# Kernel optimization log

Hardware: AMD Instinct MI355X
Metric: run time of the kernel (lower is better)

## Reference

```python
import jax, jax.numpy as jnp
import numpy as np


def _make_grid(h, w, stride=1):
    """Vectorized port of gen_grid_coordinates_exp. Returns (1, 3*Ho, 3*Wo, 2) float32,
    last dim = (x_norm, y_norm) in [-1,1] (torch grid_sample convention)."""
    rows = np.arange(0, h, stride)
    cols = np.arange(0, w, stride)
    theta = -((rows + 0.5) / h * np.pi - np.pi / 2)          # (Ho,)
    phi = (cols + 0.5) / w * 2 * np.pi - np.pi               # (Wo,)
    dtheta = np.pi / h
    dphi = 2 * np.pi / w
    # 3x3 tangent-plane offsets (du: horizontal, dv: vertical), per get_exp_duv
    du = np.tan(dphi) * np.array([[-1., 0., 1.]] * 3)                      # (3,3)
    dv = np.tan(dtheta) * np.array([[1., 1., 1.], [0., 0., 0.], [-1., -1., -1.]])
    T = theta[:, None, None, None]   # (Ho,1,1,1)
    P = phi[None, :, None, None]     # (1,Wo,1,1)
    u_x = -du * np.sin(P) - dv * np.sin(T) * np.cos(P)       # (Ho,Wo,3,3)
    u_y = du * np.cos(P) - dv * np.sin(T) * np.sin(P)
    u_z = dv * np.cos(T) + np.zeros_like(u_x)
    u_norm = np.sqrt(u_x ** 2 + u_y ** 2 + u_z ** 2)
    u_div = np.where(u_norm == 0, 1.0, u_norm)
    c, s = np.cos(u_norm), np.sin(u_norm)
    ex = np.cos(T) * np.cos(P) * c + u_x / u_div * s
    ey = np.cos(T) * np.sin(P) * c + u_y / u_div * s
    ez = np.sin(T) * c + u_z / u_div * s
    new_phi = np.arctan2(ey, ex)
    new_theta = np.arcsin(np.clip(ez, -1.0, 1.0))
    new_r = (-new_theta + np.pi / 2) * h / np.pi - 0.5
    new_c = ((new_phi + np.pi) * w / (2 * np.pi) - 0.5 + w) % w
    # kernel center samples the original integer pixel exactly
    new_r[:, :, 1, 1] = rows[:, None]
    new_c[:, :, 1, 1] = cols[None, :]
    gx = new_c * 2.0 / w - 1.0
    gy = new_r * 2.0 / h - 1.0
    grid = np.stack([gx, gy], axis=-1)                        # (Ho,Wo,3,3,2)
    Ho, Wo = len(rows), len(cols)
    grid = grid.transpose(0, 2, 1, 3, 4).reshape(1, Ho * 3, Wo * 3, 2)
    return grid.astype(np.float32)


def _grid_sample_bilinear(x, grid):
    """torch.nn.functional.grid_sample(mode='bilinear', padding='zeros', align_corners=False).
    x: (B,C,H,W); grid: (1,Hg,Wg,2) shared across batch."""
    B, C, H, W = x.shape
    gx = grid[0, ..., 0]
    gy = grid[0, ..., 1]
    Hg, Wg = gx.shape
    ix = ((gx + 1.0) * W - 1.0) * 0.5   # unnormalize, align_corners=False
    iy = ((gy + 1.0) * H - 1.0) * 0.5
    x0 = jnp.floor(ix); x1 = x0 + 1.0
    y0 = jnp.floor(iy); y1 = y0 + 1.0
    xf = x.reshape(B, C, H * W)

    def corner(xc, yc, wgt):
        valid = (xc >= 0) & (xc < W) & (yc >= 0) & (yc < H)
        xi = jnp.clip(xc, 0, W - 1).astype(jnp.int32)
        yi = jnp.clip(yc, 0, H - 1).astype(jnp.int32)
        idx = (yi * W + xi).reshape(-1)                      # (Hg*Wg,)
        w_eff = (wgt * valid.astype(wgt.dtype)).reshape(-1)  # zero-pad OOB
        return xf[:, :, idx] * w_eff                          # (B,C,Hg*Wg)

    out = (corner(x0, y0, (x1 - ix) * (y1 - iy))
           + corner(x1, y0, (ix - x0) * (y1 - iy))
           + corner(x0, y1, (x1 - ix) * (iy - y0))
           + corner(x1, y1, (ix - x0) * (iy - y0)))
    return out.reshape(B, C, Hg, Wg)


def setup_inputs() -> dict:
    key = jax.random.key(0)
    k1, k2 = jax.random.split(key)
    B, Cin, Cout, H, W = 4, 128, 256, 128, 256
    x = jax.random.normal(k1, (B, Cin, H, W), dtype=jnp.float32)
    # kaiming_uniform_(a=sqrt(5)) -> U(-1/sqrt(fan_in), 1/sqrt(fan_in)), fan_in = Cin*9
    bound = 1.0 / np.sqrt(Cin * 9)
    weight = jax.random.uniform(k2, (Cout, Cin, 3, 3), dtype=jnp.float32,
                                minval=-bound, maxval=bound)
    bias = jnp.zeros((Cout,), dtype=jnp.float32)
    grid = jnp.asarray(_make_grid(H, W, stride=1))  # (1, 3H, 3W, 2)
    return {"x": x, "weight": weight, "bias": bias, "grid": grid}


def reference(x, weight, bias, grid):
    sampled = _grid_sample_bilinear(x, grid)                 # (B,C,3H,3W)
    out = jax.lax.conv_general_dilated(
        sampled, weight, window_strides=(3, 3), padding='VALID',
        dimension_numbers=('NCHW', 'OIHW', 'NCHW'))          # (B,Cout,H,W)
    return out + bias[None, :, None, None]
```

## Files before the change

kernel.cpp:

```cpp
#include <hip/hip_runtime.h>


#define Hh   128
#define Ww   256
#define HWp  (Hh*Ww)
#define CIN  128
#define COUT 256
#define KTOT 1152
#define NPTS (384*768)
#define BM   64
#define BN   256
#define BK   32
#define NKS  (KTOT/BK)

typedef __attribute__((ext_vector_type(8))) _Float16 f16x8;
typedef __attribute__((ext_vector_type(4))) float    f32x4;

__device__ __forceinline__ f16x8 bcast8(float f) {
    _Float16 h = (_Float16)f;
    f16x8 v;
#pragma unroll
    for (int i = 0; i < 8; ++i) v[i] = h;
    return v;
}

__global__ void prep(const float* __restrict__ grid, const float* __restrict__ w,
                     const float* __restrict__ x,
                     int2* __restrict__ tI, float4* __restrict__ tW,
                     _Float16* __restrict__ wt2, _Float16* __restrict__ xt) {
    const int bid = blockIdx.x;
    const int t   = threadIdx.x;
    if (bid < NPTS / 256) {
        int g = bid * 256 + t;
        int hh = g / 768, ww = g - hh * 768;
        int ho = hh / 3, ii = hh - 3 * ho;
        int wo = ww / 3, jj = ww - 3 * wo;

        float gx = grid[2 * g + 0];
        float gy = grid[2 * g + 1];
        float ix = ((gx + 1.0f) * (float)Ww - 1.0f) * 0.5f;
        float iy = ((gy + 1.0f) * (float)Hh - 1.0f) * 0.5f;
        float x0f = floorf(ix), y0f = floorf(iy);
        int x0 = (int)x0f, y0 = (int)y0f;
        float wx1 = ix - x0f, wx0 = 1.0f - wx1;
        float wy1 = iy - y0f, wy0 = 1.0f - wy1;

        float wyt = (y0 >= 0 && y0 < Hh) ? wy0 : 0.0f;
        float wyb = (y0 + 1 >= 0 && y0 + 1 < Hh) ? wy1 : 0.0f;
        int r0 = min(max(y0, 0), Hh - 1);
        int r1 = min(max(y0 + 1, 0), Hh - 1);

        int xb; float cw0, cw1;
        if (x0 < 0)            { xb = 0;      cw0 = wx1; cw1 = 0.0f; }
        else if (x0 > Ww - 2)  { xb = Ww - 2; cw0 = 0.0f; cw1 = wx0; }
        else                   { xb = x0;     cw0 = wx0; cw1 = wx1; }

        int e = (ho * Ww + wo) * 9 + ii * 3 + jj;
        tI[e] = make_int2(r0 * Ww + xb, r1 * Ww + xb);
        tW[e] = make_float4(cw0 * wyt, cw1 * wyt, cw0 * wyb, cw1 * wyb);
    } else if (bid < 2 * (NPTS / 256)) {
        int o = (bid - NPTS / 256) * 256 + t;
        int kk = o & (BK - 1);
        int n  = (o >> 5) & (COUT - 1);
        int ks = o >> 13;
        int ij = ks % 9;
        int ci = (ks / 9) * 32 + kk;
        wt2[o] = (_Float16)w[n * KTOT + ci * 9 + ij];
    } else {
        int r   = (bid - 2 * (NPTS / 256)) * 256 + t;
        int sp4 = (r & 8191) * 4;
        int cg  = (r >> 13) & 15;
        int b   = r >> 17;
        const float* src = x + ((size_t)(b * CIN + cg * 8)) * HWp + sp4;
        float4 v[8];
#pragma unroll
        for (int j = 0; j < 8; ++j) v[j] = *(const float4*)(src + (size_t)j * HWp);
#pragma unroll
        for (int s = 0; s < 4; ++s) {
            f16x8 ov;
#pragma unroll
            for (int j = 0; j < 8; ++j) ov[j] = (_Float16)((&v[j].x)[s]);
            *(f16x8*)&xt[((size_t)(b * HWp + sp4 + s)) * CIN + cg * 8] = ov;
        }
    }
}

__global__ __launch_bounds__(512, 4) void sphconv_gemm(
    const _Float16* __restrict__ xt, const _Float16* __restrict__ wt2,
    const float* __restrict__ bias, const int2* __restrict__ tI,
    const float4* __restrict__ tW, float* __restrict__ out) {

    __shared__ int2   sTI[9 * BM];
    __shared__ float4 sTW[9 * BM];
    __shared__ __align__(16) _Float16 sA[2][BM * 40];

    const int t = threadIdx.x;
    const int bid = blockIdx.x;
    const int swz = (bid & 7) * 256 + (bid >> 3);
    const int m0  = swz * BM;
    const int b   = m0 >> 15;
    const int sp0 = m0 & (HWp - 1);
    const _Float16* xb_ = xt + (size_t)b * (HWp * CIN);

    for (int e = t; e < 9 * BM; e += 512) {
        int r = e & (BM - 1), ij = e >> 6;
        sTI[e] = tI[(sp0 + r) * 9 + ij];
        sTW[e] = tW[(sp0 + r) * 9 + ij];
    }

    const int lane = t & 63;
    const int wid  = t >> 6;
    const int wrow = wid >> 2;
    const int wcol = wid & 3;
    const int quad = lane >> 4;
    const int l16  = lane & 15;

    const bool isA = (t < 256);
    const int  mr  = t & 63;
    const int  chb = ((t >> 6) & 3) * 8;

    const _Float16* wfrag = wt2 + (wcol * 64 + l16) * BK + quad * 8;

    f32x4 acc[2][4];
#pragma unroll
    for (int r = 0; r < 2; ++r)
#pragma unroll
        for (int c = 0; c < 4; ++c) {
            f32x4 z = {0.0f, 0.0f, 0.0f, 0.0f};
            acc[r][c] = z;
        }

    __syncthreads();

    f16x8 bc[4], bn[4];
    if (isA) {
        const int2   o  = sTI[mr];
        const float4 wv = sTW[mr];
        const _Float16* p = xb_ + (size_t)o.x * CIN + chb;
        const _Float16* q = xb_ + (size_t)o.y * CIN + chb;
        f16x8 av = (*(const f16x8*)p)         * bcast8(wv.x)
                 + (*(const f16x8*)(p + CIN)) * bcast8(wv.y)
                 + (*(const f16x8*)q)         * bcast8(wv.z)
                 + (*(const f16x8*)(q + CIN)) * bcast8(wv.w);
        *(f16x8*)&sA[0][mr * 40 + chb] = av;
    }
#pragma unroll
    for (int c = 0; c < 4; ++c)
        bc[c] = *(const f16x8*)(wfrag + c * 16 * BK);
    __syncthreads();

#define STEP_BODY(KS, CURA, NXTA, BCUR, BNXT)                                   \
    {                                                                           \
        const int  ks_   = (KS);                                                \
        const bool have_ = (ks_ + 1 < NKS);                                     \
        f16x8 p00, p01, p10, p11;                                               \
        float4 wv;                                                              \
        if (isA && have_) {                                                     \
            const int ij2 = (ks_ + 1) % 9;                                      \
            const int cb2 = ((ks_ + 1) / 9) * 32;                               \
            const int2 o = sTI[ij2 * BM + mr];                                  \
            wv = sTW[ij2 * BM + mr];                                            \
            const _Float16* p = xb_ + (size_t)o.x * CIN + cb2 + chb;            \
            const _Float16* q = xb_ + (size_t)o.y * CIN + cb2 + chb;            \
            p00 = *(const f16x8*)p;  p01 = *(const f16x8*)(p + CIN);            \
            p10 = *(const f16x8*)q;  p11 = *(const f16x8*)(q + CIN);            \
        }                                                                       \
        if (have_) {                                                            \
            const _Float16* src = wfrag + (size_t)(ks_ + 1) * (COUT * BK);      \
            _Pragma("unroll")                                                   \
            for (int c = 0; c < 4; ++c)                                         \
                BNXT[c] = *(const f16x8*)(src + c * 16 * BK);                   \
        }                                                                       \
        f16x8 af[2];                                                            \
        _Pragma("unroll")                                                       \
        for (int r = 0; r < 2; ++r)                                             \
            af[r] = *(const f16x8*)(&CURA[(wrow * 32 + r * 16 + l16) * 40 +     \
                                          quad * 8]);                           \
        _Pragma("unroll")                                                       \
        for (int r = 0; r < 2; ++r)                                             \
            _Pragma("unroll")                                                   \
            for (int c = 0; c < 4; ++c)                                         \
                acc[r][c] = __builtin_amdgcn_mfma_f32_16x16x32_f16(             \
                    af[r], BCUR[c], acc[r][c], 0, 0, 0);                        \
        if (isA && have_) {                                                     \
            f16x8 av = p00 * bcast8(wv.x) + p01 * bcast8(wv.y)                  \
                     + p10 * bcast8(wv.z) + p11 * bcast8(wv.w);                 \
            *(f16x8*)&NXTA[mr * 40 + chb] = av;                                 \
        }                                                                       \
        __syncthreads();                                                        \
    }

    for (int ks = 0; ks < NKS; ks += 2) {
        STEP_BODY(ks,     sA[0], sA[1], bc, bn)
        STEP_BODY(ks + 1, sA[1], sA[0], bn, bc)
    }
#undef STEP_BODY

#pragma unroll
    for (int c = 0; c < 4; ++c) {
        int n = wcol * 64 + c * 16 + l16;
        float bv = bias[n];
        float* outn = out + (((size_t)(b * COUT + n)) << 15) + sp0;
#pragma unroll
        for (int r = 0; r < 2; ++r) {
            int mbase = wrow * 32 + r * 16 + quad * 4;
            float4 v = make_float4(acc[r][c][0] + bv, acc[r][c][1] + bv,
                                   acc[r][c][2] + bv, acc[r][c][3] + bv);
            *(float4*)(&outn[mbase]) = v;
        }
    }
}

extern "C" void kernel_launch(void* const* d_in, const int* in_sizes, int n_in,
                              void* d_out, int out_size, void* d_ws, size_t ws_size,
                              hipStream_t stream) {
    const float* x    = (const float*)d_in[0];
    const float* w    = (const float*)d_in[1];
    const float* bias = (const float*)d_in[2];
    const float* grid = (const float*)d_in[3];
    float* out = (float*)d_out;

    char* ws = (char*)d_ws;
    int2*     tI  = (int2*)(ws);
    float4*   tW  = (float4*)(ws + 2359296);
    _Float16* wt2 = (_Float16*)(ws + 7077888);
    _Float16* xt  = (_Float16*)(ws + 7667712);

    prep<<<1152 + 1152 + 2048, 256, 0, stream>>>(grid, w, x, tI, tW, wt2, xt);
    sphconv_gemm<<<(4 * HWp) / BM, 512, 0, stream>>>(xt, wt2, bias, tI, tW, out);
}
```

Measured before the change: 485.6 us.

## Double K-step per barrier and remap warps to full-M tiles

The GEMM main loop now handles two BK=32 slices per barrier, with a 64x72 shared A tile, so the number of __syncthreads is halved. All 512 threads gather A (each thread group takes one of the two k-slices), where before only half did. Each warp now owns all 64 rows and a 32-column slice of N, reading four A fragments from LDS per k-half. A manual lgkmcnt wait with s_barrier and sched_barrier replaces __syncthreads. The cost is more registers for prefetched B and A, and more LDS reads per warp.

```diff
diff --git a/kernel.cpp b/kernel.cpp
--- a/kernel.cpp
+++ b/kernel.cpp
@@ -12,6 +12,7 @@
 #define BN   256
 #define BK   32
 #define NKS  (KTOT/BK)
+#define NSS  (NKS/2)
 
 typedef __attribute__((ext_vector_type(8))) _Float16 f16x8;
 typedef __attribute__((ext_vector_type(4))) float    f32x4;
@@ -92,7 +93,7 @@
 
     __shared__ int2   sTI[9 * BM];
     __shared__ float4 sTW[9 * BM];
-    __shared__ __align__(16) _Float16 sA[2][BM * 40];
+    __shared__ __align__(16) _Float16 sA[2][BM * 72];
 
     const int t = threadIdx.x;
     const int bid = blockIdx.x;
@@ -110,100 +111,107 @@
 
     const int lane = t & 63;
     const int wid  = t >> 6;
-    const int wrow = wid >> 2;
-    const int wcol = wid & 3;
+    const int wcol = wid;
     const int quad = lane >> 4;
     const int l16  = lane & 15;
-
-    const bool isA = (t < 256);
-    const int  mr  = t & 63;
-    const int  chb = ((t >> 6) & 3) * 8;
-
-    const _Float16* wfrag = wt2 + (wcol * 64 + l16) * BK + quad * 8;
-
-    f32x4 acc[2][4];
-#pragma unroll
-    for (int r = 0; r < 2; ++r)
-#pragma unroll
-        for (int c = 0; c < 4; ++c) {
+    const int qk   = quad * 8;
+
+    const int row = t & 63;
+    const int chb = ((t >> 6) & 3) * 8;
+    const int g   = t >> 8;
+
+    const int wb = (wcol * 32 + l16) * BK + qk;
+
+    f32x4 acc[4][2];
+#pragma unroll
+    for (int r = 0; r < 4; ++r)
+#pragma unroll
+        for (int c = 0; c < 2; ++c) {
             f32x4 z = {0.0f, 0.0f, 0.0f, 0.0f};
             acc[r][c] = z;
         }
 
     __syncthreads();
 
-    f16x8 bc[4], bn[4];
-    if (isA) {
-        const int2   o  = sTI[mr];
-        const float4 wv = sTW[mr];
+    f16x8 bcA[4], bcB[4];
+    {
+        const int2   o  = sTI[g * BM + row];
+        const float4 wv = sTW[g * BM + row];
         const _Float16* p = xb_ + (size_t)o.x * CIN + chb;
         const _Float16* q = xb_ + (size_t)o.y * CIN + chb;
         f16x8 av = (*(const f16x8*)p)         * bcast8(wv.x)
                  + (*(const f16x8*)(p + CIN)) * bcast8(wv.y)
                  + (*(const f16x8*)q)         * bcast8(wv.z)
                  + (*(const f16x8*)(q + CIN)) * bcast8(wv.w);
-        *(f16x8*)&sA[0][mr * 40 + chb] = av;
-    }
-#pragma unroll
-    for (int c = 0; c < 4; ++c)
-        bc[c] = *(const f16x8*)(wfrag + c * 16 * BK);
+        *(f16x8*)&sA[0][row * 72 + g * 32 + chb] = av;
+        const _Float16* ws0 = wt2 + wb;
+        bcA[0] = *(const f16x8*)(ws0);
+        bcA[1] = *(const f16x8*)(ws0 + 16 * BK);
+        bcA[2] = *(const f16x8*)(ws0 + COUT * BK);
+        bcA[3] = *(const f16x8*)(ws0 + COUT * BK + 16 * BK);
+    }
     __syncthreads();
 
-#define STEP_BODY(KS, CURA, NXTA, BCUR, BNXT)                                   \
+#define SUPER(S, CUR, NXT, BC, BN)                                              \
     {                                                                           \
-        const int  ks_   = (KS);                                                \
-        const bool have_ = (ks_ + 1 < NKS);                                     \
+        const bool have_ = ((S) + 1 < NSS);                                     \
         f16x8 p00, p01, p10, p11;                                               \
-        float4 wv;                                                              \
-        if (isA && have_) {                                                     \
-            const int ij2 = (ks_ + 1) % 9;                                      \
-            const int cb2 = ((ks_ + 1) / 9) * 32;                               \
-            const int2 o = sTI[ij2 * BM + mr];                                  \
-            wv = sTW[ij2 * BM + mr];                                            \
-            const _Float16* p = xb_ + (size_t)o.x * CIN + cb2 + chb;            \
-            const _Float16* q = xb_ + (size_t)o.y * CIN + cb2 + chb;            \
+        float4 wvn;                                                             \
+        if (have_) {                                                            \
+            const int mk  = 2 * ((S) + 1) + g;                                  \
+            const int ijn = mk % 9;                                             \
+            const int cbn = (mk / 9) * 32;                                      \
+            const int2 o  = sTI[ijn * BM + row];                                \
+            wvn = sTW[ijn * BM + row];                                          \
+            const _Float16* p = xb_ + (size_t)o.x * CIN + cbn + chb;            \
+            const _Float16* q = xb_ + (size_t)o.y * CIN + cbn + chb;            \
             p00 = *(const f16x8*)p;  p01 = *(const f16x8*)(p + CIN);            \
             p10 = *(const f16x8*)q;  p11 = *(const f16x8*)(q + CIN);            \
+            const _Float16* ws_ = wt2 + (size_t)(2 * ((S) + 1)) * (COUT * BK)   \
+                                      + wb;                                     \
+            BN[0] = *(const f16x8*)(ws_);                                       \
+            BN[1] = *(const f16x8*)(ws_ + 16 * BK);                             \
+            BN[2] = *(const f16x8*)(ws_ + COUT * BK);                           \
+            BN[3] = *(const f16x8*)(ws_ + COUT * BK + 16 * BK);                 \
+        }                                                                       \
+        _Pragma("unroll")                                                       \
+        for (int kh = 0; kh < 2; ++kh) {                                        \
+            f16x8 af[4];                                                        \
+            _Pragma("unroll")                                                   \
+            for (int r = 0; r < 4; ++r)                                         \
+                af[r] = *(const f16x8*)(&CUR[(r * 16 + l16) * 72 +              \
+                                             kh * 32 + qk]);                    \
+            _Pragma("unroll")                                                   \
+            for (int r = 0; r < 4; ++r)                                         \
+                _Pragma("unroll")                                               \
+                for (int c = 0; c < 2; ++c)                                     \
+                    acc[r][c] = __builtin_amdgcn_mfma_f32_16x16x32_f16(         \
+                        af[r], BC[kh * 2 + c], acc[r][c], 0, 0, 0);             \
         }                                                                       \
         if (have_) {                                                            \
-            const _Float16* src = wfrag + (size_t)(ks_ + 1) * (COUT * BK);      \
-            _Pragma("unroll")                                                   \
-            for (int c = 0; c < 4; ++c)                                         \
-                BNXT[c] = *(const f16x8*)(src + c * 16 * BK);                   \
+            f16x8 av = p00 * bcast8(wvn.x) + p01 * bcast8(wvn.y)                \
+                     + p10 * bcast8(wvn.z) + p11 * bcast8(wvn.w);               \
+            *(f16x8*)&NXT[row * 72 + g * 32 + chb] = av;                        \
         }                                                                       \
-        f16x8 af[2];                                                            \
-        _Pragma("unroll")                                                       \
-        for (int r = 0; r < 2; ++r)                                             \
-            af[r] = *(const f16x8*)(&CURA[(wrow * 32 + r * 16 + l16) * 40 +     \
-                                          quad * 8]);                           \
-        _Pragma("unroll")                                                       \
-        for (int r = 0; r < 2; ++r)                                             \
-            _Pragma("unroll")                                                   \
-            for (int c = 0; c < 4; ++c)                                         \
-                acc[r][c] = __builtin_amdgcn_mfma_f32_16x16x32_f16(             \
-                    af[r], BCUR[c], acc[r][c], 0, 0, 0);                        \
-        if (isA && have_) {                                                     \
-            f16x8 av = p00 * bcast8(wv.x) + p01 * bcast8(wv.y)                  \
-                     + p10 * bcast8(wv.z) + p11 * bcast8(wv.w);                 \
-            *(f16x8*)&NXTA[mr * 40 + chb] = av;                                 \
-        }                                                                       \
-        __syncthreads();                                                        \
-    }
-
-    for (int ks = 0; ks < NKS; ks += 2) {
-        STEP_BODY(ks,     sA[0], sA[1], bc, bn)
-        STEP_BODY(ks + 1, sA[1], sA[0], bn, bc)
-    }
-#undef STEP_BODY
-
-#pragma unroll
-    for (int c = 0; c < 4; ++c) {
-        int n = wcol * 64 + c * 16 + l16;
+        asm volatile("s_waitcnt lgkmcnt(0)" ::: "memory");                      \
+        __builtin_amdgcn_s_barrier();                                           \
+        __builtin_amdgcn_sched_barrier(0);                                      \
+    }
+
+    for (int s = 0; s < NSS; s += 2) {
+        SUPER(s,     sA[0], sA[1], bcA, bcB)
+        SUPER(s + 1, sA[1], sA[0], bcB, bcA)
+    }
+#undef SUPER
+
+#pragma unroll
+    for (int c = 0; c < 2; ++c) {
+        int n = wcol * 32 + c * 16 + l16;
         float bv = bias[n];
         float* outn = out + (((size_t)(b * COUT + n)) << 15) + sp0;
 #pragma unroll
-        for (int r = 0; r < 2; ++r) {
-            int mbase = wrow * 32 + r * 16 + quad * 4;
+        for (int r = 0; r < 4; ++r) {
+            int mbase = r * 16 + quad * 4;
             float4 v = make_float4(acc[r][c][0] + bv, acc[r][c][1] + bv,
                                    acc[r][c][2] + bv, acc[r][c][3] + bv);
             *(float4*)(&outn[mbase]) = v;
```

After: 446.9 us. 8.0% less time.
